# Performance work log

Hardware: AMD Instinct MI355X
Metric: run time of the kernel (lower is better)

Reference implementation:

```python
import jax, jax.numpy as jnp
import numpy as np
from jax import lax

PRUNE_RATE = 0.5  # k: fraction of weights KEPT


def setup_inputs() -> dict:
    key = jax.random.key(0)
    ks = jax.random.split(key, 11)
    B = 512
    inp = {
        "x": jax.random.normal(ks[0], (B, 3, 32, 32), dtype=jnp.float32),
        # weights (kaiming-ish scale)
        "w1": jax.random.normal(ks[1], (64, 3, 3, 3), dtype=jnp.float32) * 0.1,
        "w2": jax.random.normal(ks[2], (64, 64, 3, 3), dtype=jnp.float32) * 0.05,
        "f1": jax.random.normal(ks[3], (256, 64 * 16 * 16), dtype=jnp.float32) * 0.01,
        "f2": jax.random.normal(ks[4], (256, 256), dtype=jnp.float32) * 0.06,
        "f3": jax.random.normal(ks[5], (10, 256), dtype=jnp.float32) * 0.06,
        # popup scores, same shapes as weights
        "s1": jax.random.normal(ks[6], (64, 3, 3, 3), dtype=jnp.float32),
        "s2": jax.random.normal(ks[7], (64, 64, 3, 3), dtype=jnp.float32),
        "s3": jax.random.normal(ks[8], (256, 64 * 16 * 16), dtype=jnp.float32),
        "s4": jax.random.normal(ks[9], (256, 256), dtype=jnp.float32),
        "s5": jax.random.normal(ks[10], (10, 256), dtype=jnp.float32),
    }
    return inp


def get_subnet(score_abs_list, k):
    """Global top-k binary masks over concatenated |scores|, STE through |scores|."""
    flat = jnp.concatenate([jnp.ravel(lax.stop_gradient(s)) for s in score_abs_list])
    n = flat.shape[0]
    j = int((1.0 - k) * n)  # number of weights zeroed
    idx = jnp.argsort(flat)
    hard = jnp.zeros((n,), flat.dtype).at[idx[j:]].set(1.0)
    masks, off = [], 0
    for s in score_abs_list:
        sz = int(np.prod(s.shape))
        h = hard[off:off + sz].reshape(s.shape)
        # straight-through: forward = hard mask, backward = identity wrt |scores|
        masks.append(s + lax.stop_gradient(h - s))
        off += sz
    return masks


def conv3x3(x, w):
    return lax.conv_general_dilated(
        x, w, window_strides=(1, 1), padding=((1, 1), (1, 1)),
        dimension_numbers=("NCHW", "OIHW", "NCHW"))


def maxpool2x2(x):
    return lax.reduce_window(x, -jnp.inf, lax.max,
                             (1, 1, 2, 2), (1, 1, 2, 2), "VALID")


def reference(x, w1, w2, f1, f2, f3, s1, s2, s3, s4, s5):
    m1, m2, m3, m4, m5 = get_subnet(
        [jnp.abs(s1), jnp.abs(s2), jnp.abs(s3), jnp.abs(s4), jnp.abs(s5)],
        PRUNE_RATE)
    out = jax.nn.relu(conv3x3(x, w1 * m1))        # [B,64,32,32]
    out = jax.nn.relu(conv3x3(out, w2 * m2))      # [B,64,32,32]
    out = maxpool2x2(out)                          # [B,64,16,16]
    out = out.reshape(out.shape[0], 64 * 16 * 16)
    out = jax.nn.relu(out @ (f1 * m3).T)           # [B,256]
    out = jax.nn.relu(out @ (f2 * m4).T)           # [B,256]
    out = out @ (f3 * m5).T                        # [B,10]
    return jnp.squeeze(out)
```

## Files before the change

### kernel.cpp

```cpp
#include <hip/hip_runtime.h>
#include <stdint.h>

typedef unsigned int u32;
typedef unsigned short u16;
typedef short short8 __attribute__((ext_vector_type(8)));
typedef float f32x4 __attribute__((ext_vector_type(4)));

#define NTOT  4300992
#define JRANK 2150496u

#define SO1 0
#define SO2 1728
#define SO3 38592
#define SO4 4232896
#define SO5 4298432

#define P_BIN    0
#define P_JP     1
#define P_TBITS  3
#define P_R      4
#define P_TIECNT 5
#define P_CUT    6

#define WS_HIST1      0u
#define WS_HIST2      16384u
#define WS_COARSE     2113536u
#define WS_PARAMS     2117632u
#define WS_ZERO_BYTES 2117888u
#define WS_TIES       2117888u
#define WS_WM         4194304u
#define WS_ACTA       33554432u
#define WS_ACTBH      167772160u
#define WS_ACTBL      184549376u
#define WS_PART       201326592u
#define WS_ACTC       205520896u
#define WS_ACTD       206045184u

#define TIE_CAP 8192

__device__ __forceinline__ float load_seg(int i, const float* a1, const float* a2,
                                          const float* a3, const float* a4, const float* a5) {
  if (i < SO2) return a1[i];
  if (i < SO3) return a2[i - SO2];
  if (i < SO4) return a3[i - SO3];
  if (i < SO5) return a4[i - SO4];
  return a5[i - SO5];
}

__device__ __forceinline__ u32 absbits(float v) {
  return __float_as_uint(v) & 0x7FFFFFFFu;
}

__device__ __forceinline__ u16 bf16rne(float f) {
  u32 u = __float_as_uint(f);
  u32 r = (u + 0x7FFFu + ((u >> 16) & 1u)) >> 16;
  return (u16)r;
}
__device__ __forceinline__ float bf16tof(u16 h) {
  return __uint_as_float(((u32)h) << 16);
}

__global__ __launch_bounds__(256) void k_hist1(const float* s1, const float* s2, const float* s3,
                                               const float* s4, const float* s5, u32* hist1) {
  __shared__ u32 h[4096];
  for (int i = threadIdx.x; i < 4096; i += 256) h[i] = 0;
  __syncthreads();
  int stride = gridDim.x * blockDim.x;
  for (int i = blockIdx.x * 256 + threadIdx.x; i < NTOT; i += stride) {
    u32 b = absbits(load_seg(i, s1, s2, s3, s4, s5)) >> 19;
    atomicAdd(&h[b], 1u);
  }
  __syncthreads();
  for (int i = threadIdx.x; i < 4096; i += 256) {
    u32 c = h[i];
    if (c) atomicAdd(&hist1[i], c);
  }
}

__global__ __launch_bounds__(1024) void k_scan1(const u32* hist1, u32* params) {
  __shared__ u32 sc[1024];
  int t = threadIdx.x;
  u32 loc[4];
  u32 own = 0;
#pragma unroll
  for (int i = 0; i < 4; i++) { loc[i] = hist1[t * 4 + i]; own += loc[i]; }
  sc[t] = own; __syncthreads();
  for (int off = 1; off < 1024; off <<= 1) {
    u32 add = (t >= off) ? sc[t - off] : 0;
    __syncthreads();
    sc[t] += add;
    __syncthreads();
  }
  u32 incl = sc[t], excl = incl - own;
  if (JRANK >= excl && JRANK < incl) {
    u32 run = excl;
#pragma unroll
    for (int i = 0; i < 4; i++) {
      if (JRANK < run + loc[i]) { params[P_BIN] = (u32)(t * 4 + i); params[P_JP] = JRANK - run; break; }
      run += loc[i];
    }
  }
}

__global__ __launch_bounds__(256) void k_hist2(const float* s1, const float* s2, const float* s3,
                                               const float* s4, const float* s5,
                                               const u32* params, u32* hist2) {
  u32 bsel = params[P_BIN];
  int stride = gridDim.x * blockDim.x;
  for (int i = blockIdx.x * 256 + threadIdx.x; i < NTOT; i += stride) {
    u32 b = absbits(load_seg(i, s1, s2, s3, s4, s5));
    if ((b >> 19) == bsel) atomicAdd(&hist2[b & 0x7FFFFu], 1u);
  }
}

__global__ __launch_bounds__(256) void k_coarse(const u32* hist2, u32* coarse) {
  __shared__ u32 red[256];
  int blk = blockIdx.x;
  u32 s = hist2[blk * 512 + threadIdx.x] + hist2[blk * 512 + 256 + threadIdx.x];
  red[threadIdx.x] = s; __syncthreads();
  for (int off = 128; off > 0; off >>= 1) {
    if (threadIdx.x < off) red[threadIdx.x] += red[threadIdx.x + off];
    __syncthreads();
  }
  if (threadIdx.x == 0) coarse[blk] = red[0];
}

__global__ __launch_bounds__(1024) void k_scan2(const u32* hist2, const u32* coarse, u32* params) {
  __shared__ u32 sc[1024];
  __shared__ u32 s_seg, s_base;
  int t = threadIdx.x;
  u32 jp = params[P_JP];
  u32 own = coarse[t];
  sc[t] = own; __syncthreads();
  for (int off = 1; off < 1024; off <<= 1) {
    u32 add = (t >= off) ? sc[t - off] : 0;
    __syncthreads();
    sc[t] += add;
    __syncthreads();
  }
  u32 incl = sc[t], excl = incl - own;
  if (jp >= excl && jp < incl) { s_seg = (u32)t; s_base = excl; }
  __syncthreads();
  u32 seg = s_seg, base = s_base, tgt = jp - base;
  u32 own2 = (t < 512) ? hist2[seg * 512 + t] : 0;
  __syncthreads();
  sc[t] = own2; __syncthreads();
  for (int off = 1; off < 1024; off <<= 1) {
    u32 add = (t >= off) ? sc[t - off] : 0;
    __syncthreads();
    sc[t] += add;
    __syncthreads();
  }
  u32 incl2 = sc[t], excl2 = incl2 - own2;
  if (t < 512 && tgt >= excl2 && tgt < incl2) {
    u32 b = params[P_BIN];
    params[P_TBITS] = (b << 19) | (seg * 512 + (u32)t);
    params[P_R] = tgt - excl2;
  }
}

__global__ __launch_bounds__(256) void k_tie(const float* s1, const float* s2, const float* s3,
                                             const float* s4, const float* s5,
                                             u32* params, u32* ties) {
  u32 tb = params[P_TBITS];
  int stride = gridDim.x * blockDim.x;
  for (int i = blockIdx.x * 256 + threadIdx.x; i < NTOT; i += stride) {
    if (absbits(load_seg(i, s1, s2, s3, s4, s5)) == tb) {
      u32 pos = atomicAdd(&params[P_TIECNT], 1u);
      if (pos < TIE_CAP) ties[pos] = (u32)i;
    }
  }
}

__global__ void k_cut(u32* params, const u32* ties) {
  if (threadIdx.x != 0 || blockIdx.x != 0) return;
  u32 m = params[P_TIECNT]; if (m > TIE_CAP) m = TIE_CAP;
  u32 r = params[P_R];
  u32 cut;
  if (r == 0) cut = 0u;
  else if (r >= m) cut = 0xFFFFFFFFu;
  else {
    long long last = -1;
    for (u32 s = 0; s < r; s++) {
      u32 cur = 0xFFFFFFFFu;
      for (u32 k = 0; k < m; k++) {
        u32 v = ties[k];
        if ((long long)v > last && v < cur) cur = v;
      }
      last = (long long)cur;
    }
    cut = (u32)(last + 1);
  }
  params[P_CUT] = cut;
}

__global__ __launch_bounds__(256) void k_mask(const float* s1, const float* s2, const float* s3,
                                              const float* s4, const float* s5,
                                              const float* w1, const float* w2, const float* w3,
                                              const float* w4, const float* w5,
                                              const u32* params, float* wm) {
  u32 tb = params[P_TBITS];
  u32 cut = params[P_CUT];
  int stride = gridDim.x * blockDim.x;
  for (int i = blockIdx.x * 256 + threadIdx.x; i < NTOT; i += stride) {
    u32 b = absbits(load_seg(i, s1, s2, s3, s4, s5));
    bool keep = (b > tb) || (b == tb && (u32)i >= cut);
    wm[i] = keep ? load_seg(i, w1, w2, w3, w4, w5) : 0.0f;
  }
}

__global__ __launch_bounds__(256) void k_conv1(const float* __restrict__ x,
                                               const float* __restrict__ wm1,
                                               u32* __restrict__ actA2) {
  __shared__ float xs[3][34][35];
  __shared__ float ws[64][27];
  int b = blockIdx.x;
  int tid = threadIdx.x;
  for (int i = tid; i < 3 * 34 * 35; i += 256) ((float*)xs)[i] = 0.0f;
  for (int i = tid; i < 1728; i += 256) ((float*)ws)[i] = wm1[i];
  __syncthreads();
  const float4* xp = (const float4*)(x + (size_t)b * 3072);
  for (int i = tid; i < 768; i += 256) {
    float4 v = xp[i];
    int c = i >> 8, p = i & 255, r = p >> 3, c4 = p & 7;
    float* dst = &xs[c][r + 1][c4 * 4 + 1];
    dst[0] = v.x; dst[1] = v.y; dst[2] = v.z; dst[3] = v.w;
  }
  __syncthreads();
  int och = tid >> 7, y = (tid >> 2) & 31, xg = tid & 3, x0 = xg * 8;
  for (int q = 0; q < 8; q++) {
    int ocb = och * 32 + q * 4;
    float acc[4][8];
#pragma unroll
    for (int o = 0; o < 4; o++)
#pragma unroll
      for (int p = 0; p < 8; p++) acc[o][p] = 0.0f;
    for (int c = 0; c < 3; c++) {
      float in[3][10];
#pragma unroll
      for (int dy = 0; dy < 3; dy++)
#pragma unroll
        for (int d = 0; d < 10; d++) in[dy][d] = xs[c][y + dy][x0 + d];
#pragma unroll
      for (int o = 0; o < 4; o++) {
#pragma unroll
        for (int ky = 0; ky < 3; ky++)
#pragma unroll
          for (int kx = 0; kx < 3; kx++) {
            float wv = ws[ocb + o][c * 9 + ky * 3 + kx];
#pragma unroll
            for (int px = 0; px < 8; px++) acc[o][px] += wv * in[ky][px + kx];
          }
      }
    }
#pragma unroll
    for (int o = 0; o < 4; o++) {
      u32 w8[8];
#pragma unroll
      for (int px = 0; px < 8; px++) {
        float v = fmaxf(acc[o][px], 0.f);
        u16 h = bf16rne(v);
        u16 lo = bf16rne(v - bf16tof(h));
        w8[px] = (u32)h | ((u32)lo << 16);
      }
      uint4* dst = (uint4*)(actA2 + (((size_t)(b * 64 + ocb + o)) << 10) + (y << 5) + x0);
      dst[0] = make_uint4(w8[0], w8[1], w8[2], w8[3]);
      dst[1] = make_uint4(w8[4], w8[5], w8[6], w8[7]);
    }
  }
}

__global__ __launch_bounds__(256, 1) void k_conv2(const u32* __restrict__ actA2,
                                                  const float* __restrict__ wm2,
                                                  u16* __restrict__ actBhi,
                                                  u16* __restrict__ actBlo) {
  __shared__ __align__(16) u16 xh[6 * 34 * 64];
  __shared__ __align__(16) u16 xl[6 * 34 * 64];
  __shared__ __align__(16) u16 wh[9 * 32 * 64];
  __shared__ __align__(16) u16 wl[9 * 32 * 64];
  int blk = blockIdx.x;
  int img = blk >> 1, oc0 = (blk & 1) * 32;
  int tid = threadIdx.x;

  for (int i = tid; i < 9 * 32 * 64; i += 256) {
    int row = i >> 6;
    int ocl = row & 31, ic = i & 63, s = row >> 5;
    float v = wm2[(size_t)(oc0 + ocl) * 576 + ic * 9 + s];
    u16 h = bf16rne(v);
    u16 lo = bf16rne(v - bf16tof(h));
    int e = ((2 * ic) ^ ((row & 7) << 4)) >> 1;
    wh[row * 64 + e] = h;
    wl[row * 64 + e] = lo;
  }

  const u32* src = actA2 + (size_t)img * 65536;
  int wv = tid >> 6, l = tid & 63;
  int pr = wv & 1, xb = wv >> 1;
  int ln15 = l & 15, lh = l >> 4;
  const f32x4 vzero = {0.f, 0.f, 0.f, 0.f};

  for (int band = 0; band < 8; band++) {
    int r0 = band * 4;
    __syncthreads();
    for (int i = tid; i < 6 * 34 * 64; i += 256) {
      int row = i >> 6, ic = i & 63;
      int yloc = row / 34;
      int xidx = row - yloc * 34;
      int iny = r0 - 1 + yloc, inx = xidx - 1;
      u32 v = 0;
      if (iny >= 0 && iny < 32 && inx >= 0 && inx < 32)
        v = src[ic * 1024 + iny * 32 + inx];
      int e = ((2 * ic) ^ ((row & 7) << 4)) >> 1;
      xh[row * 64 + e] = (u16)(v & 0xFFFFu);
      xl[row * 64 + e] = (u16)(v >> 16);
    }
    __syncthreads();

    f32x4 acc[2][2];
#pragma unroll
    for (int mi = 0; mi < 2; mi++)
#pragma unroll
      for (int t = 0; t < 2; t++) acc[mi][t] = vzero;

#pragma unroll
    for (int ky = 0; ky < 3; ky++) {
#pragma unroll
      for (int kx = 0; kx < 3; kx++) {
        int s = 3 * ky + kx;
#pragma unroll
        for (int c = 0; c < 2; c++) {
          int bb = 64 * c + lh * 16;
          int rb0 = s * 32 + ln15;
          int rb1 = rb0 + 16;
          short8 bh0 = *(const short8*)&wh[rb0 * 64 + ((bb ^ ((rb0 & 7) << 4)) >> 1)];
          short8 bl0 = *(const short8*)&wl[rb0 * 64 + ((bb ^ ((rb0 & 7) << 4)) >> 1)];
          short8 bh1 = *(const short8*)&wh[rb1 * 64 + ((bb ^ ((rb1 & 7) << 4)) >> 1)];
          short8 bl1 = *(const short8*)&wl[rb1 * 64 + ((bb ^ ((rb1 & 7) << 4)) >> 1)];
#pragma unroll
          for (int mi = 0; mi < 2; mi++) {
            int ra = (2 * pr + mi + ky) * 34 + xb * 16 + ln15 + kx;
            short8 ah = *(const short8*)&xh[ra * 64 + ((bb ^ ((ra & 7) << 4)) >> 1)];
            short8 al = *(const short8*)&xl[ra * 64 + ((bb ^ ((ra & 7) << 4)) >> 1)];
            acc[mi][0] = __builtin_amdgcn_mfma_f32_16x16x32_bf16(ah, bh0, acc[mi][0], 0, 0, 0);
            acc[mi][0] = __builtin_amdgcn_mfma_f32_16x16x32_bf16(ah, bl0, acc[mi][0], 0, 0, 0);
            acc[mi][0] = __builtin_amdgcn_mfma_f32_16x16x32_bf16(al, bh0, acc[mi][0], 0, 0, 0);
            acc[mi][1] = __builtin_amdgcn_mfma_f32_16x16x32_bf16(ah, bh1, acc[mi][1], 0, 0, 0);
            acc[mi][1] = __builtin_amdgcn_mfma_f32_16x16x32_bf16(ah, bl1, acc[mi][1], 0, 0, 0);
            acc[mi][1] = __builtin_amdgcn_mfma_f32_16x16x32_bf16(al, bh1, acc[mi][1], 0, 0, 0);
          }
        }
      }
    }

    int py = band * 2 + pr;
#pragma unroll
    for (int tau = 0; tau < 2; tau++) {
      int oc = oc0 + tau * 16 + ln15;
      size_t obase = ((size_t)img * 64 + oc) * 256 + py * 16;
#pragma unroll
      for (int u = 0; u < 2; u++) {
        int g = 2 * u;
        float a = fmaxf(fmaxf(acc[0][tau][g], acc[0][tau][g + 1]),
                        fmaxf(acc[1][tau][g], acc[1][tau][g + 1]));
        a = fmaxf(a, 0.0f);
        u16 h = bf16rne(a);
        u16 lo = bf16rne(a - bf16tof(h));
        int px = xb * 8 + lh * 2 + u;
        actBhi[obase + px] = h;
        actBlo[obase + px] = lo;
      }
    }
  }
}

__global__ __launch_bounds__(256) void k_fc1(const u16* __restrict__ Ahi,
                                             const u16* __restrict__ Alo,
                                             const float* __restrict__ f1m,
                                             float* __restrict__ part) {
  __shared__ __align__(16) u16 Ash[64 * 40];
  __shared__ __align__(16) u16 Asl[64 * 40];
  __shared__ __align__(16) u16 Bsh[64 * 40];
  __shared__ __align__(16) u16 Bsl[64 * 40];
  int blk = blockIdx.x;
  int ks = blk >> 5, ms = (blk >> 2) & 7, ns = blk & 3;
  int m0 = ms * 64, n0 = ns * 64, kbase = ks * 2048;
  int tid = threadIdx.x;
  int wv = tid >> 6, l = tid & 63, ln15 = l & 15, lh = l >> 4;
  const f32x4 vzero = {0.f, 0.f, 0.f, 0.f};
  f32x4 acc[4];
#pragma unroll
  for (int i = 0; i < 4; i++) acc[i] = vzero;

  for (int step = 0; step < 64; step++) {
    int k0 = kbase + step * 32;
    __syncthreads();
    for (int i = tid; i < 2048; i += 256) {
      int m = i >> 5, kk = i & 31;
      size_t ga = (size_t)(m0 + m) * 16384 + k0 + kk;
      Ash[m * 40 + kk] = Ahi[ga];
      Asl[m * 40 + kk] = Alo[ga];
      float v = f1m[(size_t)(n0 + m) * 16384 + k0 + kk];
      u16 h = bf16rne(v);
      Bsh[m * 40 + kk] = h;
      Bsl[m * 40 + kk] = bf16rne(v - bf16tof(h));
    }
    __syncthreads();
    int rb = wv * 16 + ln15;
    short8 bh = *(const short8*)&Bsh[rb * 40 + lh * 8];
    short8 bl = *(const short8*)&Bsl[rb * 40 + lh * 8];
#pragma unroll
    for (int mu = 0; mu < 4; mu++) {
      int ra = mu * 16 + ln15;
      short8 ah = *(const short8*)&Ash[ra * 40 + lh * 8];
      short8 al = *(const short8*)&Asl[ra * 40 + lh * 8];
      acc[mu] = __builtin_amdgcn_mfma_f32_16x16x32_bf16(ah, bh, acc[mu], 0, 0, 0);
      acc[mu] = __builtin_amdgcn_mfma_f32_16x16x32_bf16(ah, bl, acc[mu], 0, 0, 0);
      acc[mu] = __builtin_amdgcn_mfma_f32_16x16x32_bf16(al, bh, acc[mu], 0, 0, 0);
    }
  }
  float* dst = part + (size_t)ks * 131072;
#pragma unroll
  for (int mu = 0; mu < 4; mu++) {
#pragma unroll
    for (int g = 0; g < 4; g++) {
      int m = m0 + mu * 16 + lh * 4 + g;
      dst[(size_t)m * 256 + n0 + wv * 16 + ln15] = acc[mu][g];
    }
  }
}

__global__ __launch_bounds__(256) void k_fc1fin(const float* __restrict__ part,
                                                float* __restrict__ actC) {
  int i = blockIdx.x * 256 + threadIdx.x;
  float s = 0.0f;
#pragma unroll
  for (int ks = 0; ks < 8; ks++) s += part[(size_t)ks * 131072 + i];
  actC[i] = fmaxf(s, 0.0f);
}

__global__ __launch_bounds__(256) void k_fc2(const float* __restrict__ actC,
                                             const float* __restrict__ f2m,
                                             float* __restrict__ actD) {
  __shared__ float c1[256];
  int b = blockIdx.x, tid = threadIdx.x;
  c1[tid] = actC[(size_t)b * 256 + tid];
  __syncthreads();
  const float4* wrow = (const float4*)(f2m + (size_t)tid * 256);
  float acc = 0.0f;
#pragma unroll 4
  for (int k4 = 0; k4 < 64; k4++) {
    float4 w = wrow[k4];
    acc += c1[k4 * 4 + 0] * w.x + c1[k4 * 4 + 1] * w.y +
           c1[k4 * 4 + 2] * w.z + c1[k4 * 4 + 3] * w.w;
  }
  actD[(size_t)b * 256 + tid] = fmaxf(acc, 0.0f);
}

__global__ __launch_bounds__(256) void k_fc3(const float* __restrict__ actD,
                                             const float* __restrict__ f3m,
                                             float* __restrict__ out) {
  __shared__ float d1[256];
  int b = blockIdx.x, tid = threadIdx.x;
  d1[tid] = actD[(size_t)b * 256 + tid];
  __syncthreads();
  if (tid < 160) {
    int n = tid >> 4, ksl = tid & 15;
    const float* wr = f3m + (size_t)n * 256 + ksl * 16;
    const float* dd = &d1[ksl * 16];
    float p = 0.0f;
#pragma unroll
    for (int i = 0; i < 16; i++) p += dd[i] * wr[i];
    p += __shfl_xor(p, 8, 16);
    p += __shfl_xor(p, 4, 16);
    p += __shfl_xor(p, 2, 16);
    p += __shfl_xor(p, 1, 16);
    if (ksl == 0) out[(size_t)b * 10 + n] = p;
  }
}

extern "C" void kernel_launch(void* const* d_in, const int* in_sizes, int n_in,
                              void* d_out, int out_size, void* d_ws, size_t ws_size,
                              hipStream_t stream) {
  const float* x  = (const float*)d_in[0];
  const float* w1 = (const float*)d_in[1];
  const float* w2 = (const float*)d_in[2];
  const float* f1 = (const float*)d_in[3];
  const float* f2 = (const float*)d_in[4];
  const float* f3 = (const float*)d_in[5];
  const float* s1 = (const float*)d_in[6];
  const float* s2 = (const float*)d_in[7];
  const float* s3 = (const float*)d_in[8];
  const float* s4 = (const float*)d_in[9];
  const float* s5 = (const float*)d_in[10];

  char* ws = (char*)d_ws;
  u32* hist1  = (u32*)(ws + WS_HIST1);
  u32* hist2  = (u32*)(ws + WS_HIST2);
  u32* coarse = (u32*)(ws + WS_COARSE);
  u32* params = (u32*)(ws + WS_PARAMS);
  u32* ties   = (u32*)(ws + WS_TIES);
  float* wm   = (float*)(ws + WS_WM);
  u32* actA2  = (u32*)(ws + WS_ACTA);
  u16* actBhi = (u16*)(ws + WS_ACTBH);
  u16* actBlo = (u16*)(ws + WS_ACTBL);
  float* part = (float*)(ws + WS_PART);
  float* actC = (float*)(ws + WS_ACTC);
  float* actD = (float*)(ws + WS_ACTD);

  hipMemsetAsync(ws, 0, WS_ZERO_BYTES, stream);

  k_hist1<<<256, 256, 0, stream>>>(s1, s2, s3, s4, s5, hist1);
  k_scan1<<<1, 1024, 0, stream>>>(hist1, params);
  k_hist2<<<256, 256, 0, stream>>>(s1, s2, s3, s4, s5, params, hist2);
  k_coarse<<<1024, 256, 0, stream>>>(hist2, coarse);
  k_scan2<<<1, 1024, 0, stream>>>(hist2, coarse, params);
  k_tie<<<256, 256, 0, stream>>>(s1, s2, s3, s4, s5, params, ties);
  k_cut<<<1, 64, 0, stream>>>(params, ties);
  k_mask<<<1024, 256, 0, stream>>>(s1, s2, s3, s4, s5, w1, w2, f1, f2, f3, params, wm);

  k_conv1<<<512, 256, 0, stream>>>(x, wm + SO1, actA2);
  k_conv2<<<1024, 256, 0, stream>>>(actA2, wm + SO2, actBhi, actBlo);
  k_fc1<<<256, 256, 0, stream>>>(actBhi, actBlo, wm + SO3, part);
  k_fc1fin<<<512, 256, 0, stream>>>(part, actC);
  k_fc2<<<512, 256, 0, stream>>>(actC, wm + SO4, actD);
  k_fc3<<<512, 256, 0, stream>>>(actD, wm + SO5, (float*)d_out);
}
```

Measured before the change: 832.2 us.

## Switch activations to channel-last packed bf16 splits and prepack conv2/fc1 weights

Conv1 now writes its activation in NHWC layout with hi/lo bf16 pairs packed per channel, and is split into row bands across more blocks. Conv2 processes a whole image per block, loads input rows as vectors, and reads prepacked MFMA-ordered weights from global memory (built by a new k_wprep kernel) instead of converting them per block. The fc1 weights are split into packed bf16 hi/lo inside k_mask, so fc1 no longer converts fp32 to bf16 in its inner loop; fc1 moves to 512 threads with 64-wide K steps and vectorized loads. Byte-permute instructions unpack hi/lo fragments in registers, which adds ALU work, and the workspace layout is reorganised.

```diff
diff --git a/kernel.cpp b/kernel.cpp
--- a/kernel.cpp
+++ b/kernel.cpp
@@ -29,12 +29,14 @@
 #define WS_ZERO_BYTES 2117888u
 #define WS_TIES       2117888u
 #define WS_WM         4194304u
-#define WS_ACTA       33554432u
-#define WS_ACTBH      167772160u
-#define WS_ACTBL      184549376u
-#define WS_PART       201326592u
-#define WS_ACTC       205520896u
-#define WS_ACTD       206045184u
+#define WS_PART       (WS_WM + 4u*SO3)
+#define WS_ACTC       (WS_PART + 4194304u)
+#define WS_ACTD       (WS_ACTC + 524288u)
+#define WS_F1PK       21495808u
+#define WS_WPK        38273024u
+#define WS_ACTA       41943040u
+#define WS_ACTBH      176160768u
+#define WS_ACTBL      192937984u
 
 #define TIE_CAP 8192
 
@@ -59,6 +61,14 @@
 __device__ __forceinline__ float bf16tof(u16 h) {
   return __uint_as_float(((u32)h) << 16);
 }
+__device__ __forceinline__ u32 packsplit(float v) {
+  u16 h = bf16rne(v);
+  u16 lo = bf16rne(v - bf16tof(h));
+  return (u32)h | ((u32)lo << 16);
+}
+
+#define PERM_HI 0x05040100u
+#define PERM_LO 0x07060302u
 
 __global__ __launch_bounds__(256) void k_hist1(const float* s1, const float* s2, const float* s3,
                                                const float* s4, const float* s5, u32* hist1) {
@@ -198,127 +208,119 @@
                                               const float* s4, const float* s5,
                                               const float* w1, const float* w2, const float* w3,
                                               const float* w4, const float* w5,
-                                              const u32* params, float* wm) {
+                                              const u32* params, float* wm, u32* f1pk) {
   u32 tb = params[P_TBITS];
   u32 cut = params[P_CUT];
   int stride = gridDim.x * blockDim.x;
   for (int i = blockIdx.x * 256 + threadIdx.x; i < NTOT; i += stride) {
     u32 b = absbits(load_seg(i, s1, s2, s3, s4, s5));
     bool keep = (b > tb) || (b == tb && (u32)i >= cut);
-    wm[i] = keep ? load_seg(i, w1, w2, w3, w4, w5) : 0.0f;
-  }
-}
-
-__global__ __launch_bounds__(256) void k_conv1(const float* __restrict__ x,
-                                               const float* __restrict__ wm1,
-                                               u32* __restrict__ actA2) {
-  __shared__ float xs[3][34][35];
-  __shared__ float ws[64][27];
-  int b = blockIdx.x;
+    float v = keep ? load_seg(i, w1, w2, w3, w4, w5) : 0.0f;
+    if (i >= SO3 && i < SO4) {
+      f1pk[i - SO3] = packsplit(v);
+    } else {
+      wm[i] = v;
+    }
+  }
+}
+
+__global__ __launch_bounds__(256) void k_wprep(const float* wm2, u32* wpk) {
+  int idx = blockIdx.x * 256 + threadIdx.x;
+  if (idx >= 36864) return;
+  int j = idx & 7, l = (idx >> 3) & 63, c = (idx >> 9) & 1, tau = (idx >> 10) & 3, s = idx >> 12;
+  int ic = c * 32 + (l >> 4) * 8 + j;
+  int oc = tau * 16 + (l & 15);
+  wpk[idx] = packsplit(wm2[oc * 576 + ic * 9 + s]);
+}
+
+__global__ __launch_bounds__(256, 2) void k_conv1(const float* __restrict__ x,
+                                                  const float* __restrict__ wm1,
+                                                  u32* __restrict__ actA) {
+  __shared__ float xsm[3 * 10 * 36];
+  __shared__ float wsm[64 * 29];
+  int blk = blockIdx.x;
+  int img = blk >> 2, yb = blk & 3, y0 = yb * 8;
   int tid = threadIdx.x;
-  for (int i = tid; i < 3 * 34 * 35; i += 256) ((float*)xs)[i] = 0.0f;
-  for (int i = tid; i < 1728; i += 256) ((float*)ws)[i] = wm1[i];
-  __syncthreads();
-  const float4* xp = (const float4*)(x + (size_t)b * 3072);
-  for (int i = tid; i < 768; i += 256) {
-    float4 v = xp[i];
-    int c = i >> 8, p = i & 255, r = p >> 3, c4 = p & 7;
-    float* dst = &xs[c][r + 1][c4 * 4 + 1];
-    dst[0] = v.x; dst[1] = v.y; dst[2] = v.z; dst[3] = v.w;
-  }
-  __syncthreads();
-  int och = tid >> 7, y = (tid >> 2) & 31, xg = tid & 3, x0 = xg * 8;
-  for (int q = 0; q < 8; q++) {
-    int ocb = och * 32 + q * 4;
-    float acc[4][8];
-#pragma unroll
-    for (int o = 0; o < 4; o++)
-#pragma unroll
-      for (int p = 0; p < 8; p++) acc[o][p] = 0.0f;
-    for (int c = 0; c < 3; c++) {
-      float in[3][10];
-#pragma unroll
-      for (int dy = 0; dy < 3; dy++)
-#pragma unroll
-        for (int d = 0; d < 10; d++) in[dy][d] = xs[c][y + dy][x0 + d];
-#pragma unroll
-      for (int o = 0; o < 4; o++) {
-#pragma unroll
-        for (int ky = 0; ky < 3; ky++)
-#pragma unroll
-          for (int kx = 0; kx < 3; kx++) {
-            float wv = ws[ocb + o][c * 9 + ky * 3 + kx];
-#pragma unroll
-            for (int px = 0; px < 8; px++) acc[o][px] += wv * in[ky][px + kx];
-          }
+  for (int i = tid; i < 1728; i += 256) {
+    int oc = i / 27, k = i - oc * 27;
+    wsm[oc * 29 + k] = wm1[i];
+  }
+  for (int i = tid; i < 1020; i += 256) {
+    int c = i / 340, r = i - c * 340;
+    int yy = r / 34, xx = r - yy * 34;
+    int y = y0 - 1 + yy, xg = xx - 1;
+    float v = 0.0f;
+    if (y >= 0 && y < 32 && xg >= 0 && xg < 32)
+      v = x[(size_t)img * 3072 + c * 1024 + y * 32 + xg];
+    xsm[c * 360 + yy * 36 + xx] = v;
+  }
+  __syncthreads();
+  int q = tid & 15, p = tid >> 4;
+  int row = p >> 1, col0 = (p & 1) * 16;
+  float acc[4][16];
+#pragma unroll
+  for (int o = 0; o < 4; o++)
+#pragma unroll
+    for (int px = 0; px < 16; px++) acc[o][px] = 0.0f;
+#pragma unroll
+  for (int c = 0; c < 3; c++) {
+#pragma unroll
+    for (int ky = 0; ky < 3; ky++) {
+      float in[18];
+#pragma unroll
+      for (int d = 0; d < 18; d++) in[d] = xsm[c * 360 + (row + ky) * 36 + col0 + d];
+#pragma unroll
+      for (int kx = 0; kx < 3; kx++) {
+#pragma unroll
+        for (int o = 0; o < 4; o++) {
+          float wv = wsm[(q * 4 + o) * 29 + c * 9 + ky * 3 + kx];
+#pragma unroll
+          for (int px = 0; px < 16; px++) acc[o][px] += wv * in[px + kx];
+        }
       }
     }
-#pragma unroll
-    for (int o = 0; o < 4; o++) {
-      u32 w8[8];
-#pragma unroll
-      for (int px = 0; px < 8; px++) {
-        float v = fmaxf(acc[o][px], 0.f);
-        u16 h = bf16rne(v);
-        u16 lo = bf16rne(v - bf16tof(h));
-        w8[px] = (u32)h | ((u32)lo << 16);
-      }
-      uint4* dst = (uint4*)(actA2 + (((size_t)(b * 64 + ocb + o)) << 10) + (y << 5) + x0);
-      dst[0] = make_uint4(w8[0], w8[1], w8[2], w8[3]);
-      dst[1] = make_uint4(w8[4], w8[5], w8[6], w8[7]);
-    }
-  }
-}
-
-__global__ __launch_bounds__(256, 1) void k_conv2(const u32* __restrict__ actA2,
-                                                  const float* __restrict__ wm2,
+  }
+  int y = y0 + row;
+#pragma unroll
+  for (int px = 0; px < 16; px++) {
+    u32 w4[4];
+#pragma unroll
+    for (int o = 0; o < 4; o++) w4[o] = packsplit(fmaxf(acc[o][px], 0.0f));
+    *(uint4*)(actA + ((size_t)img * 1024 + y * 32 + col0 + px) * 64 + q * 4) =
+        make_uint4(w4[0], w4[1], w4[2], w4[3]);
+  }
+}
+
+__global__ __launch_bounds__(256, 2) void k_conv2(const u32* __restrict__ actA,
+                                                  const u32* __restrict__ wpk,
                                                   u16* __restrict__ actBhi,
                                                   u16* __restrict__ actBlo) {
-  __shared__ __align__(16) u16 xh[6 * 34 * 64];
-  __shared__ __align__(16) u16 xl[6 * 34 * 64];
-  __shared__ __align__(16) u16 wh[9 * 32 * 64];
-  __shared__ __align__(16) u16 wl[9 * 32 * 64];
-  int blk = blockIdx.x;
-  int img = blk >> 1, oc0 = (blk & 1) * 32;
+  __shared__ u32 xs[204 * 68];
+  int img = blockIdx.x;
   int tid = threadIdx.x;
-
-  for (int i = tid; i < 9 * 32 * 64; i += 256) {
-    int row = i >> 6;
-    int ocl = row & 31, ic = i & 63, s = row >> 5;
-    float v = wm2[(size_t)(oc0 + ocl) * 576 + ic * 9 + s];
-    u16 h = bf16rne(v);
-    u16 lo = bf16rne(v - bf16tof(h));
-    int e = ((2 * ic) ^ ((row & 7) << 4)) >> 1;
-    wh[row * 64 + e] = h;
-    wl[row * 64 + e] = lo;
-  }
-
-  const u32* src = actA2 + (size_t)img * 65536;
-  int wv = tid >> 6, l = tid & 63;
-  int pr = wv & 1, xb = wv >> 1;
+  int l = tid & 63, wv = tid >> 6;
+  int mh = wv & 1, nh = wv >> 1;
   int ln15 = l & 15, lh = l >> 4;
+  const u32* src = actA + (size_t)img * 65536;
   const f32x4 vzero = {0.f, 0.f, 0.f, 0.f};
 
   for (int band = 0; band < 8; band++) {
     int r0 = band * 4;
     __syncthreads();
-    for (int i = tid; i < 6 * 34 * 64; i += 256) {
-      int row = i >> 6, ic = i & 63;
-      int yloc = row / 34;
-      int xidx = row - yloc * 34;
-      int iny = r0 - 1 + yloc, inx = xidx - 1;
-      u32 v = 0;
-      if (iny >= 0 && iny < 32 && inx >= 0 && inx < 32)
-        v = src[ic * 1024 + iny * 32 + inx];
-      int e = ((2 * ic) ^ ((row & 7) << 4)) >> 1;
-      xh[row * 64 + e] = (u16)(v & 0xFFFFu);
-      xl[row * 64 + e] = (u16)(v >> 16);
-    }
-    __syncthreads();
-
-    f32x4 acc[2][2];
-#pragma unroll
-    for (int mi = 0; mi < 2; mi++)
+    for (int i = tid; i < 3264; i += 256) {
+      int row = i >> 4, q = i & 15;
+      int ry = row / 34, rx = row - ry * 34;
+      int y = r0 - 1 + ry, xg = rx - 1;
+      uint4 v = make_uint4(0, 0, 0, 0);
+      if (y >= 0 && y < 32 && xg >= 0 && xg < 32)
+        v = *(const uint4*)(src + (y * 32 + xg) * 64 + q * 4);
+      *(uint4*)&xs[row * 68 + q * 4] = v;
+    }
+    __syncthreads();
+
+    f32x4 acc[4][2];
+#pragma unroll
+    for (int mi = 0; mi < 4; mi++)
 #pragma unroll
       for (int t = 0; t < 2; t++) acc[mi][t] = vzero;
 
@@ -326,105 +328,147 @@
     for (int ky = 0; ky < 3; ky++) {
 #pragma unroll
       for (int kx = 0; kx < 3; kx++) {
-        int s = 3 * ky + kx;
+        int s = ky * 3 + kx;
 #pragma unroll
         for (int c = 0; c < 2; c++) {
-          int bb = 64 * c + lh * 16;
-          int rb0 = s * 32 + ln15;
-          int rb1 = rb0 + 16;
-          short8 bh0 = *(const short8*)&wh[rb0 * 64 + ((bb ^ ((rb0 & 7) << 4)) >> 1)];
-          short8 bl0 = *(const short8*)&wl[rb0 * 64 + ((bb ^ ((rb0 & 7) << 4)) >> 1)];
-          short8 bh1 = *(const short8*)&wh[rb1 * 64 + ((bb ^ ((rb1 & 7) << 4)) >> 1)];
-          short8 bl1 = *(const short8*)&wl[rb1 * 64 + ((bb ^ ((rb1 & 7) << 4)) >> 1)];
-#pragma unroll
-          for (int mi = 0; mi < 2; mi++) {
-            int ra = (2 * pr + mi + ky) * 34 + xb * 16 + ln15 + kx;
-            short8 ah = *(const short8*)&xh[ra * 64 + ((bb ^ ((ra & 7) << 4)) >> 1)];
-            short8 al = *(const short8*)&xl[ra * 64 + ((bb ^ ((ra & 7) << 4)) >> 1)];
-            acc[mi][0] = __builtin_amdgcn_mfma_f32_16x16x32_bf16(ah, bh0, acc[mi][0], 0, 0, 0);
-            acc[mi][0] = __builtin_amdgcn_mfma_f32_16x16x32_bf16(ah, bl0, acc[mi][0], 0, 0, 0);
-            acc[mi][0] = __builtin_amdgcn_mfma_f32_16x16x32_bf16(al, bh0, acc[mi][0], 0, 0, 0);
-            acc[mi][1] = __builtin_amdgcn_mfma_f32_16x16x32_bf16(ah, bh1, acc[mi][1], 0, 0, 0);
-            acc[mi][1] = __builtin_amdgcn_mfma_f32_16x16x32_bf16(ah, bl1, acc[mi][1], 0, 0, 0);
-            acc[mi][1] = __builtin_amdgcn_mfma_f32_16x16x32_bf16(al, bh1, acc[mi][1], 0, 0, 0);
+          const u32* wb = wpk + ((s * 4 + nh * 2) * 2 + c) * 512 + l * 8;
+          uint4 br0 = *(const uint4*)wb;
+          uint4 br1 = *(const uint4*)(wb + 4);
+          uint4 br2 = *(const uint4*)(wb + 1024);
+          uint4 br3 = *(const uint4*)(wb + 1028);
+          union { u32 u[4]; short8 s8; } bh0, bl0, bh1, bl1;
+          bh0.u[0] = __builtin_amdgcn_perm(br0.y, br0.x, PERM_HI);
+          bh0.u[1] = __builtin_amdgcn_perm(br0.w, br0.z, PERM_HI);
+          bh0.u[2] = __builtin_amdgcn_perm(br1.y, br1.x, PERM_HI);
+          bh0.u[3] = __builtin_amdgcn_perm(br1.w, br1.z, PERM_HI);
+          bl0.u[0] = __builtin_amdgcn_perm(br0.y, br0.x, PERM_LO);
+          bl0.u[1] = __builtin_amdgcn_perm(br0.w, br0.z, PERM_LO);
+          bl0.u[2] = __builtin_amdgcn_perm(br1.y, br1.x, PERM_LO);
+          bl0.u[3] = __builtin_amdgcn_perm(br1.w, br1.z, PERM_LO);
+          bh1.u[0] = __builtin_amdgcn_perm(br2.y, br2.x, PERM_HI);
+          bh1.u[1] = __builtin_amdgcn_perm(br2.w, br2.z, PERM_HI);
+          bh1.u[2] = __builtin_amdgcn_perm(br3.y, br3.x, PERM_HI);
+          bh1.u[3] = __builtin_amdgcn_perm(br3.w, br3.z, PERM_HI);
+          bl1.u[0] = __builtin_amdgcn_perm(br2.y, br2.x, PERM_LO);
+          bl1.u[1] = __builtin_amdgcn_perm(br2.w, br2.z, PERM_LO);
+          bl1.u[2] = __builtin_amdgcn_perm(br3.y, br3.x, PERM_LO);
+          bl1.u[3] = __builtin_amdgcn_perm(br3.w, br3.z, PERM_LO);
+#pragma unroll
+          for (int mi = 0; mi < 4; mi++) {
+            int row = (2 * mh + (mi >> 1) + ky) * 34 + (mi & 1) * 16 + ln15 + kx;
+            const u32* xa = &xs[row * 68 + c * 32 + lh * 8];
+            uint4 ar0 = *(const uint4*)xa;
+            uint4 ar1 = *(const uint4*)(xa + 4);
+            union { u32 u[4]; short8 s8; } ah, al;
+            ah.u[0] = __builtin_amdgcn_perm(ar0.y, ar0.x, PERM_HI);
+            ah.u[1] = __builtin_amdgcn_perm(ar0.w, ar0.z, PERM_HI);
+            ah.u[2] = __builtin_amdgcn_perm(ar1.y, ar1.x, PERM_HI);
+            ah.u[3] = __builtin_amdgcn_perm(ar1.w, ar1.z, PERM_HI);
+            al.u[0] = __builtin_amdgcn_perm(ar0.y, ar0.x, PERM_LO);
+            al.u[1] = __builtin_amdgcn_perm(ar0.w, ar0.z, PERM_LO);
+            al.u[2] = __builtin_amdgcn_perm(ar1.y, ar1.x, PERM_LO);
+            al.u[3] = __builtin_amdgcn_perm(ar1.w, ar1.z, PERM_LO);
+            acc[mi][0] = __builtin_amdgcn_mfma_f32_16x16x32_bf16(ah.s8, bh0.s8, acc[mi][0], 0, 0, 0);
+            acc[mi][0] = __builtin_amdgcn_mfma_f32_16x16x32_bf16(ah.s8, bl0.s8, acc[mi][0], 0, 0, 0);
+            acc[mi][0] = __builtin_amdgcn_mfma_f32_16x16x32_bf16(al.s8, bh0.s8, acc[mi][0], 0, 0, 0);
+            acc[mi][1] = __builtin_amdgcn_mfma_f32_16x16x32_bf16(ah.s8, bh1.s8, acc[mi][1], 0, 0, 0);
+            acc[mi][1] = __builtin_amdgcn_mfma_f32_16x16x32_bf16(ah.s8, bl1.s8, acc[mi][1], 0, 0, 0);
+            acc[mi][1] = __builtin_amdgcn_mfma_f32_16x16x32_bf16(al.s8, bh1.s8, acc[mi][1], 0, 0, 0);
           }
         }
       }
     }
 
-    int py = band * 2 + pr;
+    int py = band * 2 + mh;
 #pragma unroll
     for (int tau = 0; tau < 2; tau++) {
-      int oc = oc0 + tau * 16 + ln15;
-      size_t obase = ((size_t)img * 64 + oc) * 256 + py * 16;
-#pragma unroll
-      for (int u = 0; u < 2; u++) {
-        int g = 2 * u;
-        float a = fmaxf(fmaxf(acc[0][tau][g], acc[0][tau][g + 1]),
-                        fmaxf(acc[1][tau][g], acc[1][tau][g + 1]));
-        a = fmaxf(a, 0.0f);
-        u16 h = bf16rne(a);
-        u16 lo = bf16rne(a - bf16tof(h));
-        int px = xb * 8 + lh * 2 + u;
-        actBhi[obase + px] = h;
-        actBlo[obase + px] = lo;
+      int oc = nh * 32 + tau * 16 + ln15;
+      size_t ob = ((size_t)img * 64 + oc) * 256 + py * 16;
+#pragma unroll
+      for (int xh2 = 0; xh2 < 2; xh2++) {
+#pragma unroll
+        for (int u = 0; u < 2; u++) {
+          float a = fmaxf(fmaxf(acc[xh2][tau][2 * u], acc[xh2][tau][2 * u + 1]),
+                          fmaxf(acc[xh2 + 2][tau][2 * u], acc[xh2 + 2][tau][2 * u + 1]));
+          a = fmaxf(a, 0.0f);
+          u16 h = bf16rne(a);
+          u16 lo = bf16rne(a - bf16tof(h));
+          int pxo = xh2 * 8 + lh * 2 + u;
+          actBhi[ob + pxo] = h;
+          actBlo[ob + pxo] = lo;
+        }
       }
     }
   }
 }
 
-__global__ __launch_bounds__(256) void k_fc1(const u16* __restrict__ Ahi,
-                                             const u16* __restrict__ Alo,
-                                             const float* __restrict__ f1m,
-                                             float* __restrict__ part) {
-  __shared__ __align__(16) u16 Ash[64 * 40];
-  __shared__ __align__(16) u16 Asl[64 * 40];
-  __shared__ __align__(16) u16 Bsh[64 * 40];
-  __shared__ __align__(16) u16 Bsl[64 * 40];
+__global__ __launch_bounds__(512, 1) void k_fc1(const u16* __restrict__ Ahi,
+                                                const u16* __restrict__ Alo,
+                                                const u32* __restrict__ f1pk,
+                                                float* __restrict__ part) {
+  __shared__ u16 Ash[64 * 72];
+  __shared__ u16 Asl[64 * 72];
+  __shared__ u32 Bs[64 * 68];
   int blk = blockIdx.x;
   int ks = blk >> 5, ms = (blk >> 2) & 7, ns = blk & 3;
   int m0 = ms * 64, n0 = ns * 64, kbase = ks * 2048;
   int tid = threadIdx.x;
-  int wv = tid >> 6, l = tid & 63, ln15 = l & 15, lh = l >> 4;
+  int l = tid & 63, wv = tid >> 6;
+  int mh = wv & 1, nh = wv >> 1;
+  int ln15 = l & 15, lh = l >> 4;
   const f32x4 vzero = {0.f, 0.f, 0.f, 0.f};
-  f32x4 acc[4];
-#pragma unroll
-  for (int i = 0; i < 4; i++) acc[i] = vzero;
-
-  for (int step = 0; step < 64; step++) {
-    int k0 = kbase + step * 32;
-    __syncthreads();
-    for (int i = tid; i < 2048; i += 256) {
-      int m = i >> 5, kk = i & 31;
-      size_t ga = (size_t)(m0 + m) * 16384 + k0 + kk;
-      Ash[m * 40 + kk] = Ahi[ga];
-      Asl[m * 40 + kk] = Alo[ga];
-      float v = f1m[(size_t)(n0 + m) * 16384 + k0 + kk];
-      u16 h = bf16rne(v);
-      Bsh[m * 40 + kk] = h;
-      Bsl[m * 40 + kk] = bf16rne(v - bf16tof(h));
-    }
-    __syncthreads();
-    int rb = wv * 16 + ln15;
-    short8 bh = *(const short8*)&Bsh[rb * 40 + lh * 8];
-    short8 bl = *(const short8*)&Bsl[rb * 40 + lh * 8];
-#pragma unroll
-    for (int mu = 0; mu < 4; mu++) {
-      int ra = mu * 16 + ln15;
-      short8 ah = *(const short8*)&Ash[ra * 40 + lh * 8];
-      short8 al = *(const short8*)&Asl[ra * 40 + lh * 8];
-      acc[mu] = __builtin_amdgcn_mfma_f32_16x16x32_bf16(ah, bh, acc[mu], 0, 0, 0);
-      acc[mu] = __builtin_amdgcn_mfma_f32_16x16x32_bf16(ah, bl, acc[mu], 0, 0, 0);
-      acc[mu] = __builtin_amdgcn_mfma_f32_16x16x32_bf16(al, bh, acc[mu], 0, 0, 0);
+  f32x4 acc[2];
+  acc[0] = vzero; acc[1] = vzero;
+
+  for (int step = 0; step < 32; step++) {
+    int k0 = kbase + step * 64;
+    __syncthreads();
+    {
+      int m = tid >> 3, kq = tid & 7;
+      size_t ga = (size_t)(m0 + m) * 16384 + k0 + kq * 8;
+      *(uint4*)&Ash[m * 72 + kq * 8] = *(const uint4*)(Ahi + ga);
+      *(uint4*)&Asl[m * 72 + kq * 8] = *(const uint4*)(Alo + ga);
+    }
+#pragma unroll
+    for (int rep = 0; rep < 2; rep++) {
+      int i = tid + rep * 512;
+      int n = i >> 4, kq = i & 15;
+      *(uint4*)&Bs[n * 68 + kq * 4] = *(const uint4*)(f1pk + (size_t)(n0 + n) * 16384 + k0 + kq * 4);
+    }
+    __syncthreads();
+#pragma unroll
+    for (int c = 0; c < 2; c++) {
+      const u32* bb = &Bs[(nh * 16 + ln15) * 68 + c * 32 + lh * 8];
+      uint4 br0 = *(const uint4*)bb;
+      uint4 br1 = *(const uint4*)(bb + 4);
+      union { u32 u[4]; short8 s8; } bh, bl;
+      bh.u[0] = __builtin_amdgcn_perm(br0.y, br0.x, PERM_HI);
+      bh.u[1] = __builtin_amdgcn_perm(br0.w, br0.z, PERM_HI);
+      bh.u[2] = __builtin_amdgcn_perm(br1.y, br1.x, PERM_HI);
+      bh.u[3] = __builtin_amdgcn_perm(br1.w, br1.z, PERM_HI);
+      bl.u[0] = __builtin_amdgcn_perm(br0.y, br0.x, PERM_LO);
+      bl.u[1] = __builtin_amdgcn_perm(br0.w, br0.z, PERM_LO);
+      bl.u[2] = __builtin_amdgcn_perm(br1.y, br1.x, PERM_LO);
+      bl.u[3] = __builtin_amdgcn_perm(br1.w, br1.z, PERM_LO);
+#pragma unroll
+      for (int mt = 0; mt < 2; mt++) {
+        int ra = ((mh * 2 + mt) * 16 + ln15) * 72 + c * 32 + lh * 8;
+        union { uint4 q; short8 s8; } ah, al;
+        ah.q = *(const uint4*)&Ash[ra];
+        al.q = *(const uint4*)&Asl[ra];
+        acc[mt] = __builtin_amdgcn_mfma_f32_16x16x32_bf16(ah.s8, bh.s8, acc[mt], 0, 0, 0);
+        acc[mt] = __builtin_amdgcn_mfma_f32_16x16x32_bf16(ah.s8, bl.s8, acc[mt], 0, 0, 0);
+        acc[mt] = __builtin_amdgcn_mfma_f32_16x16x32_bf16(al.s8, bh.s8, acc[mt], 0, 0, 0);
+      }
     }
   }
   float* dst = part + (size_t)ks * 131072;
 #pragma unroll
-  for (int mu = 0; mu < 4; mu++) {
+  for (int mt = 0; mt < 2; mt++) {
 #pragma unroll
     for (int g = 0; g < 4; g++) {
-      int m = m0 + mu * 16 + lh * 4 + g;
-      dst[(size_t)m * 256 + n0 + wv * 16 + ln15] = acc[mu][g];
+      int m = m0 + (mh * 2 + mt) * 16 + lh * 4 + g;
+      dst[(size_t)m * 256 + n0 + nh * 16 + ln15] = acc[mt][g];
     }
   }
 }
@@ -500,7 +544,9 @@
   u32* params = (u32*)(ws + WS_PARAMS);
   u32* ties   = (u32*)(ws + WS_TIES);
   float* wm   = (float*)(ws + WS_WM);
-  u32* actA2  = (u32*)(ws + WS_ACTA);
+  u32* f1pk   = (u32*)(ws + WS_F1PK);
+  u32* wpk    = (u32*)(ws + WS_WPK);
+  u32* actA   = (u32*)(ws + WS_ACTA);
   u16* actBhi = (u16*)(ws + WS_ACTBH);
   u16* actBlo = (u16*)(ws + WS_ACTBL);
   float* part = (float*)(ws + WS_PART);
@@ -516,11 +562,12 @@
   k_scan2<<<1, 1024, 0, stream>>>(hist2, coarse, params);
   k_tie<<<256, 256, 0, stream>>>(s1, s2, s3, s4, s5, params, ties);
   k_cut<<<1, 64, 0, stream>>>(params, ties);
-  k_mask<<<1024, 256, 0, stream>>>(s1, s2, s3, s4, s5, w1, w2, f1, f2, f3, params, wm);
-
-  k_conv1<<<512, 256, 0, stream>>>(x, wm + SO1, actA2);
-  k_conv2<<<1024, 256, 0, stream>>>(actA2, wm + SO2, actBhi, actBlo);
-  k_fc1<<<256, 256, 0, stream>>>(actBhi, actBlo, wm + SO3, part);
+  k_mask<<<1024, 256, 0, stream>>>(s1, s2, s3, s4, s5, w1, w2, f1, f2, f3, params, wm, f1pk);
+
+  k_wprep<<<144, 256, 0, stream>>>(wm + SO2, wpk);
+  k_conv1<<<2048, 256, 0, stream>>>(x, wm + SO1, actA);
+  k_conv2<<<512, 256, 0, stream>>>(actA, wpk, actBhi, actBlo);
+  k_fc1<<<256, 512, 0, stream>>>(actBhi, actBlo, f1pk, part);
   k_fc1fin<<<512, 256, 0, stream>>>(part, actC);
   k_fc2<<<512, 256, 0, stream>>>(actC, wm + SO4, actD);
   k_fc3<<<512, 256, 0, stream>>>(actD, wm + SO5, (float*)d_out);
```

New measurement: 678.2 us. 18.5% less time.
